# Performance work log

Hardware: AMD Instinct MI355X
Metric: run time of the kernel (lower is better)

Reference implementation:

```python
import jax, jax.numpy as jnp
import numpy as np

N_NODES = 100000
NEG_SLOPE = 0.2


def gat_conv(x, W, att_src, att_dst, bias, src, dst, heads, out_ch):
    # x: [N, F_in]; W: [F_in, heads*out_ch]; att_*: [heads, out_ch]; bias: [heads*out_ch]
    N = x.shape[0]
    h = (x @ W).reshape(N, heads, out_ch)                 # [N, H, C]
    a_src = jnp.sum(h * att_src[None], axis=-1)           # [N, H]
    a_dst = jnp.sum(h * att_dst[None], axis=-1)           # [N, H]
    # per-edge unnormalized attention logits (PyG GATConv)
    alpha = jax.nn.leaky_relu(a_src[src] + a_dst[dst], NEG_SLOPE)   # [E, H]
    # scatter-softmax over edges grouped by destination node
    m = jax.ops.segment_max(alpha, dst, num_segments=N)   # [N, H]
    m = jnp.where(jnp.isfinite(m), m, 0.0)
    e = jnp.exp(alpha - m[dst])                           # [E, H]
    s = jax.ops.segment_sum(e, dst, num_segments=N)       # [N, H]
    alpha = e / (s[dst] + 1e-16)
    # weighted scatter-add aggregation of neighbor features
    out = jax.ops.segment_sum(alpha[:, :, None] * h[src], dst, num_segments=N)  # [N, H, C]
    return out.reshape(N, heads * out_ch) + bias


def setup_inputs() -> dict:
    key = jax.random.key(0)
    ks = jax.random.split(key, 10)
    F_in = 128
    x = jax.random.normal(ks[0], (N_NODES, F_in), dtype=jnp.float32)
    edge_index = jax.random.randint(ks[1], (2, 3200000), 0, N_NODES, dtype=jnp.int64)
    g = 0.1
    return {
        "x": x,
        "edge_index": edge_index,
        "W1": jax.random.normal(ks[2], (F_in, 32), jnp.float32) * g,
        "att_src1": jax.random.normal(ks[3], (2, 16), jnp.float32) * g,
        "att_dst1": jax.random.normal(ks[4], (2, 16), jnp.float32) * g,
        "b1": jnp.zeros((32,), jnp.float32),
        "W2": jax.random.normal(ks[5], (32, 2), jnp.float32) * g,
        "att_src2": jax.random.normal(ks[6], (1, 2), jnp.float32) * g,
        "att_dst2": jax.random.normal(ks[7], (1, 2), jnp.float32) * g,
        "b2": jnp.zeros((2,), jnp.float32),
    }


def reference(x, edge_index, W1, att_src1, att_dst1, b1, W2, att_src2, att_dst2, b2):
    N = x.shape[0]
    # add self-loops (PyG GATConv default add_self_loops=True)
    loops = jnp.arange(N, dtype=edge_index.dtype)
    src = jnp.concatenate([edge_index[0], loops])
    dst = jnp.concatenate([edge_index[1], loops])
    h = gat_conv(x, W1, att_src1, att_dst1, b1, src, dst, heads=2, out_ch=16)
    h = jax.nn.elu(h)
    h = gat_conv(h, W2, att_src2, att_dst2, b2, src, dst, heads=1, out_ch=2)
    return jax.nn.log_softmax(h, axis=1)
```

## Files before the change

### kernel.cpp

```cpp
#include <hip/hip_runtime.h>
#include <hip/hip_bf16.h>
#include <hip/hip_fp16.h>

#define LEAK   0.2f
#define NPB    200
#define CAP    8192
#define CAPSH  13
#define SBITS  17
#define SMASK  0x1FFFF
#define CHUNKB 8192

__device__ __forceinline__ unsigned pkh(float a, float b) {
    __half2 h = __floats2half2_rn(a, b);
    return *(unsigned*)&h;
}
__device__ __forceinline__ float2 uph(unsigned u) {
    __half2 h = *(__half2*)&u;
    return __half22float2(h);
}

__global__ __launch_bounds__(512) void kbin(const int* __restrict__ ei, int E, int K,
                                            int* __restrict__ cursor,
                                            int* __restrict__ binned) {
    __shared__ int hist[512], gb[512], lc[512];
    __shared__ int probe;
    int t = threadIdx.x;
    hist[t] = 0;
    if (t == 0) probe = 0;
    __syncthreads();
    if (t < 256) {
        int zc = 0;
#pragma unroll
        for (int j = 0; j < 4; j++) zc += (ei[(t * 4 + j) * 2 + 1] == 0) ? 1 : 0;
        if (zc) atomicAdd(&probe, zc);
    }
    __syncthreads();
    int f = (probe == 1024);
    int e0 = blockIdx.x * CHUNKB;
    int ss[16], dd[16];
#pragma unroll
    for (int i = 0; i < 16; i++) {
        int e = e0 + t + 512 * i;
        ss[i] = -1;
        dd[i] = 0;
        if (e < E) {
            int s, d;
            if (f) { s = ei[2 * e]; d = ei[2 * (e + E)]; }
            else   { s = ei[e];     d = ei[e + E]; }
            ss[i] = s;
            dd[i] = d;
            atomicAdd(&hist[d / NPB], 1);
        }
    }
    __syncthreads();
    int h = hist[t];
    lc[t] = 0;
    if (t < K && h) gb[t] = (t << CAPSH) + atomicAdd(&cursor[t], h);
    __syncthreads();
#pragma unroll
    for (int i = 0; i < 16; i++) {
        if (ss[i] >= 0) {
            int bk = dd[i] / NPB;
            int dloc = dd[i] - bk * NPB;
            int pos = atomicAdd(&lc[bk], 1);
            int gpos = gb[bk] + pos;
            if (gpos < ((bk + 1) << CAPSH))
                binned[gpos] = ss[i] | (dloc << SBITS);
        }
    }
}

__global__ __launch_bounds__(256) void k1(const float* __restrict__ x,
                                          const float* __restrict__ W1,
                                          const float* __restrict__ atts,
                                          const float* __restrict__ attd,
                                          uint2* __restrict__ h1h,
                                          float* __restrict__ a1s,
                                          float* __restrict__ a1d, int N,
                                          int* __restrict__ cursor, int K) {
    __shared__ float Ws[128 * 32];
    __shared__ float xs[64 * 132];
    int t = threadIdx.x;
    if (blockIdx.x == 0) {
        for (int u = t; u < K; u += 256) cursor[u] = 0;
    }
    const float4* W4 = (const float4*)W1;
    float4* Ws4 = (float4*)Ws;
#pragma unroll
    for (int i = 0; i < 4; i++) Ws4[t + 256 * i] = W4[t + 256 * i];
    long long node0 = (long long)blockIdx.x * 64;
    const float4* x4 = (const float4*)x;
    float4* xs4 = (float4*)xs;
#pragma unroll
    for (int i = 0; i < 8; i++) {
        int idx = t + 256 * i;
        int row = idx >> 5, col = idx & 31;
        long long n = node0 + row;
        float4 v = make_float4(0.f, 0.f, 0.f, 0.f);
        if (n < N) v = x4[n * 32 + col];
        xs4[row * 33 + col] = v;
    }
    __syncthreads();

    int cg = t & 7, ns = t >> 3;
    const float4* xr0 = (const float4*)(xs + (ns * 2) * 132);
    const float4* xr1 = (const float4*)(xs + (ns * 2 + 1) * 132);
    float acc0[4] = {0.f, 0.f, 0.f, 0.f}, acc1[4] = {0.f, 0.f, 0.f, 0.f};
#pragma unroll 8
    for (int k4 = 0; k4 < 32; k4++) {
        float4 xa = xr0[k4], xb = xr1[k4];
        float av[4] = {xa.x, xa.y, xa.z, xa.w};
        float bv[4] = {xb.x, xb.y, xb.z, xb.w};
#pragma unroll
        for (int i = 0; i < 4; i++) {
            float4 w = Ws4[(k4 * 4 + i) * 8 + cg];
            acc0[0] = fmaf(av[i], w.x, acc0[0]);
            acc0[1] = fmaf(av[i], w.y, acc0[1]);
            acc0[2] = fmaf(av[i], w.z, acc0[2]);
            acc0[3] = fmaf(av[i], w.w, acc0[3]);
            acc1[0] = fmaf(bv[i], w.x, acc1[0]);
            acc1[1] = fmaf(bv[i], w.y, acc1[1]);
            acc1[2] = fmaf(bv[i], w.z, acc1[2]);
            acc1[3] = fmaf(bv[i], w.w, acc1[3]);
        }
    }
    long long gn0 = node0 + ns * 2, gn1 = gn0 + 1;
    if (gn0 < N) h1h[gn0 * 8 + cg] = make_uint2(pkh(acc0[0], acc0[1]),
                                                pkh(acc0[2], acc0[3]));
    if (gn1 < N) h1h[gn1 * 8 + cg] = make_uint2(pkh(acc1[0], acc1[1]),
                                                pkh(acc1[2], acc1[3]));

    float ps0 = 0.f, pd0 = 0.f, ps1 = 0.f, pd1 = 0.f;
#pragma unroll
    for (int i = 0; i < 4; i++) {
        float aa = atts[cg * 4 + i], dd = attd[cg * 4 + i];
        ps0 = fmaf(acc0[i], aa, ps0);
        pd0 = fmaf(acc0[i], dd, pd0);
        ps1 = fmaf(acc1[i], aa, ps1);
        pd1 = fmaf(acc1[i], dd, pd1);
    }
#pragma unroll
    for (int m = 1; m < 4; m <<= 1) {
        ps0 += __shfl_xor(ps0, m, 64);
        pd0 += __shfl_xor(pd0, m, 64);
        ps1 += __shfl_xor(ps1, m, 64);
        pd1 += __shfl_xor(pd1, m, 64);
    }
    if ((cg & 3) == 0) {
        int hd = cg >> 2;
        if (gn0 < N) { a1s[gn0 * 2 + hd] = ps0; a1d[gn0 * 2 + hd] = pd0; }
        if (gn1 < N) { a1s[gn1 * 2 + hd] = ps1; a1d[gn1 * 2 + hd] = pd1; }
    }
}

__global__ __launch_bounds__(1024) void kfused(const int* __restrict__ cursor,
                                               const int* __restrict__ binned,
                                               const uint2* __restrict__ h1h,
                                               const float* __restrict__ a1s,
                                               const float* __restrict__ a1d,
                                               const float* __restrict__ b1,
                                               const float* __restrict__ W2,
                                               const float* __restrict__ as2,
                                               const float* __restrict__ ad2,
                                               float4* __restrict__ pk,
                                               int* __restrict__ srcs,
                                               int* __restrict__ od, int N) {
    __shared__ int lsrc[CAP];
    __shared__ int ldeg[NPB], lcur[NPB], loff[NPB];
    __shared__ int swt[4];
    int b = blockIdx.x, t = threadIdx.x;
    int node0 = b * NPB;
    int nn = min(NPB, N - node0);
    int cnt = cursor[b];
    if (cnt > CAP) cnt = CAP;
    const int* bb = binned + ((long long)b << CAPSH);
    if (t < NPB) ldeg[t] = 0;
    __syncthreads();
    int pv[8];
#pragma unroll
    for (int j = 0; j < 8; j++) {
        int i = t + 1024 * j;
        pv[j] = (i < cnt) ? bb[i] : -1;
        if (pv[j] >= 0) atomicAdd(&ldeg[pv[j] >> SBITS], 1);
    }
    __syncthreads();
    {
        int v = 0, xsc = 0;
        if (t < 256) {
            v = (t < nn) ? ldeg[t] : 0;
            xsc = v;
#pragma unroll
            for (int o = 1; o < 64; o <<= 1) {
                int y = __shfl_up(xsc, o, 64);
                if ((t & 63) >= o) xsc += y;
            }
            if ((t & 63) == 63) swt[t >> 6] = xsc;
        }
        __syncthreads();
        if (t < 256) {
            int add = 0;
#pragma unroll
            for (int j = 0; j < 4; j++)
                if (j < (t >> 6)) add += swt[j];
            xsc += add;
            if (t < nn) {
                int rel = xsc - v;
                loff[t] = rel;
                lcur[t] = rel;
                od[node0 + t] = rel | (v << 14);
            }
        }
        __syncthreads();
    }
#pragma unroll
    for (int j = 0; j < 8; j++) {
        if (pv[j] >= 0) {
            int pos = atomicAdd(&lcur[pv[j] >> SBITS], 1);
            lsrc[pos] = pv[j] & SMASK;
        }
    }
    __syncthreads();
    for (int i = t; i < cnt; i += 1024) srcs[((long long)b << CAPSH) + i] = lsrc[i];

    int wv = t >> 6, lane = t & 63;
    int e8 = lane >> 3, c4 = lane & 7, hd = c4 >> 2;
    bool wlane = (c4 & 3) == 0;
    for (int ni = wv; ni < nn; ni += 16) {
        int n = node0 + ni;
        float a1dn = a1d[2 * n + hd];
        int base = loff[ni], g = ldeg[ni];
        float4 acc = make_float4(0.f, 0.f, 0.f, 0.f);
        float wsum = 0.f;
        for (int tt = e8 - 1; tt < g; tt += 16) {
            int t2 = tt + 8;
            bool p2 = t2 < g;
            int s0 = (tt < 0) ? n : lsrc[base + tt];
            int s1 = p2 ? lsrc[base + t2] : s0;
            float as0 = a1s[2 * s0 + hd];
            float as1 = a1s[2 * s1 + hd];
            uint2 hb0 = h1h[(size_t)s0 * 8 + c4];
            uint2 hb1 = h1h[(size_t)s1 * 8 + c4];
            float al0 = as0 + a1dn;
            al0 = al0 > 0.f ? al0 : LEAK * al0;
            float w0 = __expf(al0);
            float al1 = as1 + a1dn;
            al1 = al1 > 0.f ? al1 : LEAK * al1;
            float w1 = p2 ? __expf(al1) : 0.f;
            float2 f01 = uph(hb0.x), f23 = uph(hb0.y);
            float2 g01 = uph(hb1.x), g23 = uph(hb1.y);
            acc.x = fmaf(w0, f01.x, acc.x);
            acc.y = fmaf(w0, f01.y, acc.y);
            acc.z = fmaf(w0, f23.x, acc.z);
            acc.w = fmaf(w0, f23.y, acc.w);
            acc.x = fmaf(w1, g01.x, acc.x);
            acc.y = fmaf(w1, g01.y, acc.y);
            acc.z = fmaf(w1, g23.x, acc.z);
            acc.w = fmaf(w1, g23.y, acc.w);
            if (wlane) wsum += w0 + w1;
        }
#pragma unroll
        for (int m = 8; m < 64; m <<= 1) {
            acc.x += __shfl_xor(acc.x, m, 64);
            acc.y += __shfl_xor(acc.y, m, 64);
            acc.z += __shfl_xor(acc.z, m, 64);
            acc.w += __shfl_xor(acc.w, m, 64);
            wsum += __shfl_xor(wsum, m, 64);
        }
        float wsH = __shfl(wsum, hd * 4, 64);
        float inv = 1.f / (wsH + 1e-16f);
        float4 bv = ((const float4*)b1)[c4];
        float4 t1;
        t1.x = acc.x * inv + bv.x;
        t1.y = acc.y * inv + bv.y;
        t1.z = acc.z * inv + bv.z;
        t1.w = acc.w * inv + bv.w;
        t1.x = t1.x > 0.f ? t1.x : __expf(t1.x) - 1.f;
        t1.y = t1.y > 0.f ? t1.y : __expf(t1.y) - 1.f;
        t1.z = t1.z > 0.f ? t1.z : __expf(t1.z) - 1.f;
        t1.w = t1.w > 0.f ? t1.w : __expf(t1.w) - 1.f;
        const float4* W24 = (const float4*)W2;
        float4 wA = W24[c4 * 2], wB = W24[c4 * 2 + 1];
        float p0 = t1.x * wA.x + t1.y * wA.z + t1.z * wB.x + t1.w * wB.z;
        float p1 = t1.x * wA.y + t1.y * wA.w + t1.z * wB.y + t1.w * wB.w;
#pragma unroll
        for (int m = 1; m < 8; m <<= 1) {
            p0 += __shfl_xor(p0, m, 64);
            p1 += __shfl_xor(p1, m, 64);
        }
        if (lane == 0)
            pk[n] = make_float4(p0 * as2[0] + p1 * as2[1], p0, p1,
                                p0 * ad2[0] + p1 * ad2[1]);
    }
}

__global__ __launch_bounds__(256) void kagg2(const int* __restrict__ od,
                                             const int* __restrict__ srcs,
                                             const float4* __restrict__ pk,
                                             const float* __restrict__ b2,
                                             float* __restrict__ out, int N) {
    int sub = threadIdx.x >> 5, k = threadIdx.x & 31;
    int n = blockIdx.x * 8 + sub;
    if (n >= N) return;
    float4 pn = pk[n];
    float adn = pn.w;
    int o = od[n];
    int base = ((n / NPB) << CAPSH) + (o & 16383);
    int g = o >> 14;
    float a0 = 0.f, a1v = 0.f, wsm = 0.f;
    for (int e = k - 1; e < g; e += 32) {
        float4 p = (e < 0) ? pn : pk[srcs[base + e]];
        float al = p.x + adn;
        al = al > 0.f ? al : LEAK * al;
        float w = __expf(al);
        a0 = fmaf(w, p.y, a0);
        a1v = fmaf(w, p.z, a1v);
        wsm += w;
    }
#pragma unroll
    for (int m = 1; m < 32; m <<= 1) {
        a0 += __shfl_xor(a0, m, 32);
        a1v += __shfl_xor(a1v, m, 32);
        wsm += __shfl_xor(wsm, m, 32);
    }
    if (k == 0) {
        float inv = 1.f / (wsm + 1e-16f);
        float o0 = a0 * inv + b2[0];
        float o1 = a1v * inv + b2[1];
        float mx = fmaxf(o0, o1);
        float lse = mx + __logf(__expf(o0 - mx) + __expf(o1 - mx));
        ((float2*)out)[n] = make_float2(o0 - lse, o1 - lse);
    }
}

extern "C" void kernel_launch(void* const* d_in, const int* in_sizes, int n_in,
                              void* d_out, int out_size, void* d_ws, size_t ws_size,
                              hipStream_t stream) {
    const float* x   = (const float*)d_in[0];
    const int*   ei  = (const int*)d_in[1];
    const float* W1  = (const float*)d_in[2];
    const float* as1 = (const float*)d_in[3];
    const float* ad1 = (const float*)d_in[4];
    const float* b1  = (const float*)d_in[5];
    const float* W2  = (const float*)d_in[6];
    const float* as2 = (const float*)d_in[7];
    const float* ad2 = (const float*)d_in[8];
    const float* b2  = (const float*)d_in[9];
    float* out = (float*)d_out;

    int N = out_size / 2;
    int E = in_sizes[1] / 2;
    int K = (N + NPB - 1) / NPB;

    float* wsp   = (float*)d_ws;
    float4* pk   = (float4*)wsp;
    uint2* h1h   = (uint2*)(pk + (size_t)N);
    float* a1s   = (float*)(h1h + (size_t)N * 8);
    float* a1d   = a1s + (size_t)N * 2;
    int* od      = (int*)(a1d + (size_t)N * 2);
    int* srcs    = od + N;
    int* binned  = srcs + (size_t)K * CAP;
    int* cursor  = binned + (size_t)K * CAP;

    int nblkB = (E + CHUNKB - 1) / CHUNKB;

    k1<<<(N + 63) / 64, 256, 0, stream>>>(x, W1, as1, ad1, h1h, a1s, a1d, N,
                                          cursor, K);
    kbin<<<nblkB, 512, 0, stream>>>(ei, E, K, cursor, binned);
    kfused<<<K, 1024, 0, stream>>>(cursor, binned, h1h, a1s, a1d,
                                   b1, W2, as2, ad2, pk, srcs, od, N);
    kagg2<<<(N + 7) / 8, 256, 0, stream>>>(od, srcs, pk, b2, out, N);
}
```

Measured before the change: 237.7 us.

## Stage binned edges in shared memory to coalesce global scatter writes

The binning kernel now computes a block-local prefix sum over the bucket histogram. It groups each chunk's edges by bucket in shared memory, recording each slot's bucket ID, then writes them to global memory in contiguous per-thread order. The aim is to replace scattered per-edge global stores with writes that run contiguously within each bucket. In exchange it uses about 48KB more LDS per block, adds extra barriers, and has a serial per-bucket loop to fill the bucket-ID array.

```diff
diff --git a/kernel.cpp b/kernel.cpp
--- a/kernel.cpp
+++ b/kernel.cpp
@@ -22,7 +22,10 @@
 __global__ __launch_bounds__(512) void kbin(const int* __restrict__ ei, int E, int K,
                                             int* __restrict__ cursor,
                                             int* __restrict__ binned) {
-    __shared__ int hist[512], gb[512], lc[512];
+    __shared__ int hist[512], gb[512], lbase[512], lcur[512];
+    __shared__ unsigned short rbk[CHUNKB];
+    __shared__ int sv[CHUNKB];
+    __shared__ int swt[8];
     __shared__ int probe;
     int t = threadIdx.x;
     hist[t] = 0;
@@ -53,20 +56,41 @@
         }
     }
     __syncthreads();
-    int h = hist[t];
-    lc[t] = 0;
-    if (t < K && h) gb[t] = (t << CAPSH) + atomicAdd(&cursor[t], h);
-    __syncthreads();
+    int h = (t < K) ? hist[t] : 0;
+    if (h) gb[t] = (t << CAPSH) + atomicAdd(&cursor[t], h);
+    int xsc = h;
+#pragma unroll
+    for (int o = 1; o < 64; o <<= 1) {
+        int y = __shfl_up(xsc, o, 64);
+        if ((t & 63) >= o) xsc += y;
+    }
+    if ((t & 63) == 63) swt[t >> 6] = xsc;
+    __syncthreads();
+    int add = 0;
+#pragma unroll
+    for (int j = 0; j < 8; j++)
+        if (j < (t >> 6)) add += swt[j];
+    int lb = xsc - h + add;
+    lbase[t] = lb;
+    lcur[t] = lb;
+    __syncthreads();
+    for (int j = 0; j < h; j++) rbk[lb + j] = (unsigned short)t;
 #pragma unroll
     for (int i = 0; i < 16; i++) {
         if (ss[i] >= 0) {
             int bk = dd[i] / NPB;
             int dloc = dd[i] - bk * NPB;
-            int pos = atomicAdd(&lc[bk], 1);
-            int gpos = gb[bk] + pos;
-            if (gpos < ((bk + 1) << CAPSH))
-                binned[gpos] = ss[i] | (dloc << SBITS);
-        }
+            int pos = atomicAdd(&lcur[bk], 1);
+            sv[pos] = ss[i] | (dloc << SBITS);
+        }
+    }
+    __syncthreads();
+    int tot = min(CHUNKB, E - e0);
+    for (int i = t; i < tot; i += 512) {
+        int bk = rbk[i];
+        int gpos = gb[bk] + (i - lbase[bk]);
+        if (gpos < ((bk + 1) << CAPSH))
+            binned[gpos] = sv[i];
     }
 }
 
```

Result: faster. 230.9 us (-2.8%).
